# Performance work log

Measured on AMD Instinct MI355X. Metric: run time of the kernel, lower is better.

## Reference

```python
import jax, jax.numpy as jnp
import numpy as np

B = 262144
N_FEAT = 256
N_D = 64
N_A = 64
N_OUT = N_D + N_A  # 128
N_STEPS = 3
N_STEP_DEP = 2
VBS = 1024
GAMMA = 1.3
EPS_BN = 1e-5
SQRT_HALF = float(np.sqrt(0.5))


def _xavier(key, shape):
    fan_in, fan_out = shape[-2], shape[-1]
    return (jax.random.normal(key, shape) * np.sqrt(2.0 / (fan_in + fan_out))).astype(jnp.float32)


def setup_inputs() -> dict:
    key = jax.random.key(0)
    ks = jax.random.split(key, 8)
    return {
        "x": jax.random.normal(ks[0], (B, N_FEAT), dtype=jnp.float32),
        "bn0_g": jnp.ones((N_FEAT,), jnp.float32),
        "bn0_b": jnp.zeros((N_FEAT,), jnp.float32),
        "W_sh0": _xavier(ks[1], (N_FEAT, 2 * N_OUT)),
        "g_sh0": jnp.ones((2 * N_OUT,), jnp.float32),
        "b_sh0": jnp.zeros((2 * N_OUT,), jnp.float32),
        "W_sh1": _xavier(ks[2], (N_OUT, 2 * N_OUT)),
        "g_sh1": jnp.ones((2 * N_OUT,), jnp.float32),
        "b_sh1": jnp.zeros((2 * N_OUT,), jnp.float32),
        "W_step": _xavier(ks[3], (N_STEPS, N_STEP_DEP, N_OUT, 2 * N_OUT)),
        "g_step": jnp.ones((N_STEPS, N_STEP_DEP, 2 * N_OUT), jnp.float32),
        "b_step": jnp.zeros((N_STEPS, N_STEP_DEP, 2 * N_OUT), jnp.float32),
        "W_att": _xavier(ks[4], (N_STEPS, N_A, N_FEAT)),
        "g_att": jnp.ones((N_STEPS, N_FEAT), jnp.float32),
        "b_att": jnp.zeros((N_STEPS, N_FEAT), jnp.float32),
    }


def batch_norm(x, g, b):
    # training-mode BN over the full batch (biased variance, as torch)
    mu = x.mean(0)
    var = ((x - mu) ** 2).mean(0)
    return (x - mu) * jax.lax.rsqrt(var + EPS_BN) * g + b


def ghost_bn(x, g, b):
    # split batch into virtual sub-batches of VBS and BN each chunk
    n, f = x.shape
    xr = x.reshape(n // VBS, VBS, f)
    mu = xr.mean(1, keepdims=True)
    var = ((xr - mu) ** 2).mean(1, keepdims=True)
    xn = (xr - mu) * jax.lax.rsqrt(var + EPS_BN)
    return xn.reshape(n, f) * g + b


def sparsemax(z):
    zs = jnp.flip(jnp.sort(z, axis=-1), axis=-1)      # descending
    cs = jnp.cumsum(zs, axis=-1)
    n = z.shape[-1]
    k = jnp.arange(1, n + 1, dtype=z.dtype)
    support = (k * zs > cs - 1.0).astype(z.dtype)
    kz = support.sum(-1, keepdims=True)
    idx = jnp.clip(kz - 1.0, 0.0).astype(jnp.int32)
    tau = (jnp.take_along_axis(cs, idx, axis=-1) - 1.0) / kz
    return jnp.maximum(z - tau, 0.0)


def glu(x, W, g, b):
    h = ghost_bn(x @ W, g, b)
    h1, h2 = jnp.split(h, 2, axis=-1)
    return h1 * jax.nn.sigmoid(h2)


def feat_transformer(x, W_sh0, g_sh0, b_sh0, W_sh1, g_sh1, b_sh1, Wst, gst, bst):
    h = glu(x, W_sh0, g_sh0, b_sh0)
    h = (h + glu(h, W_sh1, g_sh1, b_sh1)) * SQRT_HALF
    for j in range(N_STEP_DEP):
        h = (h + glu(h, Wst[j], gst[j], bst[j])) * SQRT_HALF
    return h


def reference(x, bn0_g, bn0_b, W_sh0, g_sh0, b_sh0, W_sh1, g_sh1, b_sh1,
              W_step, g_step, b_step, W_att, g_att, b_att):
    x_bn = batch_norm(x, bn0_g, bn0_b)
    prior = jnp.ones((B, N_FEAT), x.dtype)
    h_a = jnp.zeros((B, N_A), x.dtype)
    d_out = jnp.zeros((B, N_D), x.dtype)
    sl = jnp.asarray(0.0, x.dtype)
    masks = []
    for s in range(N_STEPS):
        a = ghost_bn(h_a @ W_att[s], g_att[s], b_att[s])
        M = sparsemax(prior * a)
        masks.append(M)
        prior = prior * (GAMMA - M)
        h = feat_transformer(M * x_bn, W_sh0, g_sh0, b_sh0, W_sh1, g_sh1, b_sh1,
                             W_step[s], g_step[s], b_step[s])
        d_out = d_out + jax.nn.relu(h[:, :N_D])
        h_a = h[:, N_D:]
        sl = sl + (-M * jnp.log(M + 1e-15)).mean()
    sl = sl / N_STEPS
    return d_out, sl, jnp.stack(masks)
```

## Files before the change

### kernel.cpp

```cpp
#include <hip/hip_runtime.h>
#include <math.h>

#define B_ROWS 262144
#define GAMMA_C 1.3f
#define EPS_C 1e-5f
#define SQH_C 0.70710678118654752440f
#define SL_SCALE (1.0f/201326592.0f)

typedef _Float16 f16;
typedef f16 f16x8 __attribute__((ext_vector_type(8)));
typedef float f32x4 __attribute__((ext_vector_type(4)));

template<int RB>
__device__ __forceinline__ unsigned swz(int row, int kb) {
  constexpr int M = (RB/16 - 1) < 31 ? (RB/16 - 1) : 31;
  return (unsigned)(row * RB + (kb ^ ((row & M) << 4)));
}

__global__ void bn0_accum(const float* __restrict__ x, float* __restrict__ sums) {
  const int col = threadIdx.x;
  const size_t r0 = (size_t)blockIdx.x * 128;
  float s1 = 0.f, s2 = 0.f;
  for (int i = 0; i < 128; ++i) {
    float v = x[(r0 + i) * 256 + col];
    s1 += v; s2 += v * v;
  }
  atomicAdd(&sums[col * 2], s1);
  atomicAdd(&sums[col * 2 + 1], s2);
}

__global__ void bn0_final(const float* __restrict__ sums, const float* __restrict__ g,
                          const float* __restrict__ b, float* __restrict__ bnA,
                          float* __restrict__ bnB) {
  int c = threadIdx.x;
  float mu = sums[c * 2] * (1.f / B_ROWS);
  float var = sums[c * 2 + 1] * (1.f / B_ROWS) - mu * mu;
  float a = rsqrtf(var + EPS_C) * g[c];
  bnA[c] = a;
  bnB[c] = b[c] - mu * a;
}

__global__ void wprep(const float* __restrict__ src, f16* __restrict__ dst, int K) {
  int idx = blockIdx.x * 256 + threadIdx.x;
  int n = idx / K, k = idx - n * K;
  dst[idx] = (f16)src[(size_t)k * 256 + n];
}

__global__ void m0_kernel(const float* __restrict__ ba, float* __restrict__ m0v,
                          float* __restrict__ prior1v, float* __restrict__ slpart) {
  const int l = threadIdx.x;
  const int c0 = l << 2;
  float z[4];
#pragma unroll
  for (int j = 0; j < 4; ++j) z[j] = ba[c0 + j];
  float m = fmaxf(fmaxf(z[0], z[1]), fmaxf(z[2], z[3]));
#pragma unroll
  for (int d = 1; d < 64; d <<= 1) m = fmaxf(m, __shfl_xor(m, d));
  float lo = m - 1.f, hi = m;
  for (int it = 0; it < 24; ++it) {
    float tau = 0.5f * (lo + hi);
    float s = fmaxf(z[0] - tau, 0.f) + fmaxf(z[1] - tau, 0.f) +
              fmaxf(z[2] - tau, 0.f) + fmaxf(z[3] - tau, 0.f);
#pragma unroll
    for (int d = 1; d < 64; d <<= 1) s += __shfl_xor(s, d);
    if (s > 1.f) lo = tau; else hi = tau;
  }
  const float tau = 0.5f * (lo + hi);
  float ent = 0.f;
#pragma unroll
  for (int j = 0; j < 4; ++j) {
    float M = fmaxf(z[j] - tau, 0.f);
    m0v[c0 + j] = M;
    prior1v[c0 + j] = GAMMA_C - M;
    ent -= M * __logf(M + 1e-15f);
  }
#pragma unroll
  for (int d = 1; d < 64; d <<= 1) ent += __shfl_xor(ent, d);
  if (l == 0) slpart[512] = ent * (262144.f * SL_SCALE);
}

__global__ void mx0_kernel(const float* __restrict__ x, const float* __restrict__ m0v,
                           const float* __restrict__ bnA, const float* __restrict__ bnB,
                           float* __restrict__ mk, f16* __restrict__ Mx) {
  __shared__ float sm[256], sa[256], sb[256];
  const int tid = threadIdx.x;
  sm[tid] = m0v[tid]; sa[tid] = bnA[tid]; sb[tid] = bnB[tid];
  __syncthreads();
  const size_t r = (size_t)blockIdx.x * 8 + (tid >> 5);
  const int c0 = (tid & 31) << 3;
  const float* xp = x + r * 256 + c0;
  f32x4 x0 = *(const f32x4*)xp;
  f32x4 x1 = *(const f32x4*)(xp + 4);
  float* mp = mk + r * 256 + c0;
  f16x8 mxv;
#pragma unroll
  for (int j = 0; j < 4; ++j) {
    mp[j] = sm[c0 + j];
    mp[4 + j] = sm[c0 + 4 + j];
    mxv[j] = (f16)(sm[c0 + j] * (x0[j] * sa[c0 + j] + sb[c0 + j]));
    mxv[4 + j] = (f16)(sm[c0 + 4 + j] * (x1[j] * sa[c0 + 4 + j] + sb[c0 + 4 + j]));
  }
  *(f16x8*)(Mx + r * 256 + c0) = mxv;
}

template <int KDIM, int VARIANT>
__launch_bounds__(1024)
__global__ void fused_glu(const f16* __restrict__ Ag, const f16* __restrict__ Wt,
                          const float* __restrict__ gv, const float* __restrict__ bv,
                          f16* __restrict__ ho, float* __restrict__ dout,
                          int first, int writeH) {
  constexpr int RC  = (KDIM == 128) ? 64 : 32;
  constexpr int NCH = 1024 / RC;
  constexpr int NRT = RC / 32;
  constexpr int KS  = KDIM / 32;
  constexpr int RB  = KDIM * 2;
  constexpr int TPR = KDIM / 8;
  __shared__ f16 sW[256 * KDIM];
  __shared__ f16 sA[RC * KDIM];
  __shared__ float sS1[256], sS2[256], sAf[256], sBf[256];
  char* sWc = (char*)sW;
  char* sAc = (char*)sA;
  const int tid = threadIdx.x;
  const int r0 = blockIdx.x << 10;
  const int w = tid >> 6, l = tid & 63, lc = l & 15, lg = l >> 4;
  const int mw = w >> 3, nw = w & 7;
  if (tid < 256) { sS1[tid] = 0.f; sS2[tid] = 0.f; }
#pragma unroll
  for (int it = 0; it < KDIM / 32; ++it) {
    int flat = it * 1024 + tid;
    int rw = flat / TPR, kc = flat % TPR;
    *(f16x8*)(sWc + swz<RB>(rw, kc * 16)) = *(const f16x8*)(Wt + rw * KDIM + kc * 8);
  }
  const int arow = tid / TPR, akc = tid % TPR;
  const f16* aB = Ag + (size_t)(r0 + arow) * KDIM + akc * 8;

  for (int pass = 0; pass < 2; ++pass) {
    float st1[2] = {0.f, 0.f}, st2[2] = {0.f, 0.f};
    f16x8 pv = *(const f16x8*)(aB);
    for (int ch = 0; ch < NCH; ++ch) {
      __syncthreads();
      *(f16x8*)(sAc + swz<RB>(arow, akc * 16)) = pv;
      __syncthreads();
      if (ch + 1 < NCH) pv = *(const f16x8*)(aB + (size_t)(ch + 1) * RC * KDIM);
      f32x4 acc[NRT][2];
#pragma unroll
      for (int i = 0; i < NRT; ++i) {
        acc[i][0] = {0.f, 0.f, 0.f, 0.f};
        acc[i][1] = {0.f, 0.f, 0.f, 0.f};
      }
#pragma unroll
      for (int ks = 0; ks < KS; ++ks) {
        f16x8 af[NRT];
#pragma unroll
        for (int i = 0; i < NRT; ++i)
          af[i] = *(const f16x8*)(sAc + swz<RB>(mw * 16 * NRT + i * 16 + lc, ks * 64 + lg * 16));
        f16x8 b0 = *(const f16x8*)(sWc + swz<RB>(nw * 16 + lc, ks * 64 + lg * 16));
        f16x8 b1 = *(const f16x8*)(sWc + swz<RB>((nw + 8) * 16 + lc, ks * 64 + lg * 16));
#pragma unroll
        for (int i = 0; i < NRT; ++i) {
          acc[i][0] = __builtin_amdgcn_mfma_f32_16x16x32_f16(af[i], b0, acc[i][0], 0, 0, 0);
          acc[i][1] = __builtin_amdgcn_mfma_f32_16x16x32_f16(af[i], b1, acc[i][1], 0, 0, 0);
        }
      }
      if (pass == 0) {
#pragma unroll
        for (int t = 0; t < 2; ++t) {
          float s1 = 0.f, s2 = 0.f;
#pragma unroll
          for (int i = 0; i < NRT; ++i)
#pragma unroll
            for (int j = 0; j < 4; ++j) { float v = acc[i][t][j]; s1 += v; s2 += v * v; }
          st1[t] += s1; st2[t] += s2;
        }
      } else {
        const int c1 = nw * 16 + lc;
        const float a1 = sAf[c1], o1 = sBf[c1], a2 = sAf[c1 + 128], o2 = sBf[c1 + 128];
#pragma unroll
        for (int i = 0; i < NRT; ++i) {
          const int rloc = mw * 16 * NRT + i * 16 + lg * 4;
          const size_t rg = (size_t)(r0 + ch * RC) + rloc;
#pragma unroll
          for (int j = 0; j < 4; ++j) {
            float g1 = acc[i][0][j] * a1 + o1;
            float g2 = acc[i][1][j] * a2 + o2;
            float hv = g1 / (1.f + __expf(-g2));
            if (VARIANT >= 1) {
              f16 hp = *(const f16*)(sAc + swz<RB>(rloc + j, c1 * 2));
              hv = (hv + (float)hp) * SQH_C;
            }
            if (VARIANT < 2 || writeH) ho[(rg + j) * 128 + c1] = (f16)hv;
            if (VARIANT == 2 && nw < 4) {
              float rl = fmaxf(hv, 0.f);
              float* dp = dout + (rg + j) * 64 + c1;
              *dp = first ? rl : (*dp + rl);
            }
          }
        }
      }
    }
    if (pass == 0) {
#pragma unroll
      for (int t = 0; t < 2; ++t) {
        float v1 = st1[t], v2 = st2[t];
        v1 += __shfl_xor(v1, 16); v2 += __shfl_xor(v2, 16);
        v1 += __shfl_xor(v1, 32); v2 += __shfl_xor(v2, 32);
        if (l < 16) {
          int c = (nw + t * 8) * 16 + lc;
          atomicAdd(&sS1[c], v1);
          atomicAdd(&sS2[c], v2);
        }
      }
      __syncthreads();
      if (tid < 256) {
        float mu = sS1[tid] * (1.f / 1024.f);
        float var = sS2[tid] * (1.f / 1024.f) - mu * mu;
        float a = rsqrtf(var + EPS_C) * gv[tid];
        sAf[tid] = a;
        sBf[tid] = bv[tid] - mu * a;
      }
    }
  }
}

template <int SMODE>
__launch_bounds__(512)
__global__ void attmask(const f16* __restrict__ h1, const f16* __restrict__ Wt,
                        const float* __restrict__ ga, const float* __restrict__ ba,
                        const float* __restrict__ bnA, const float* __restrict__ bnB,
                        const float* __restrict__ prior1v, const f16* __restrict__ prin,
                        f16* __restrict__ prout, const float* __restrict__ x,
                        float* __restrict__ mk, f16* __restrict__ Mx,
                        float* __restrict__ slpart) {
  __shared__ f16 sW[256 * 64];
  __shared__ f16 sA[128 * 64];
  __shared__ float sS1[256], sS2[256], sAf[256], sBf[256], sbA[256], sbB[256], spv[256];
  __shared__ float sEnt[8];
  char* sWc = (char*)sW;
  char* sAc = (char*)sA;
  const int tid = threadIdx.x;
  const int vb = blockIdx.x;
  const int r0 = vb << 10;
  const int w = tid >> 6, l = tid & 63, lc = l & 15, lg = l >> 4;
  if (tid < 256) {
    sS1[tid] = 0.f; sS2[tid] = 0.f;
    sbA[tid] = bnA[tid]; sbB[tid] = bnB[tid];
    if (SMODE == 1) spv[tid] = prior1v[tid];
  }
#pragma unroll
  for (int it = 0; it < 4; ++it) {
    int flat = it * 512 + tid;
    int rw = flat >> 3, kc = flat & 7;
    *(f16x8*)(sWc + swz<128>(rw, kc * 16)) = *(const f16x8*)(Wt + rw * 64 + kc * 8);
  }
  const int arow = tid >> 3, akc = tid & 7;
  const f16* aB = h1 + (size_t)(r0 + arow) * 128 + 64 + akc * 8;
  float ent = 0.f;

  for (int pass = 0; pass < 2; ++pass) {
    float st1[16], st2[16];
#pragma unroll
    for (int t = 0; t < 16; ++t) { st1[t] = 0.f; st2[t] = 0.f; }
    f16x8 pv0 = *(const f16x8*)(aB);
    f16x8 pv1 = *(const f16x8*)(aB + (size_t)64 * 128);
    for (int ch = 0; ch < 8; ++ch) {
      __syncthreads();
      *(f16x8*)(sAc + swz<128>(arow, akc * 16)) = pv0;
      *(f16x8*)(sAc + swz<128>(arow + 64, akc * 16)) = pv1;
      __syncthreads();
      if (ch + 1 < 8) {
        pv0 = *(const f16x8*)(aB + (size_t)(ch + 1) * 128 * 128);
        pv1 = *(const f16x8*)(aB + (size_t)((ch + 1) * 128 + 64) * 128);
      }
      f16x8 af0 = *(const f16x8*)(sAc + swz<128>(w * 16 + lc, lg * 16));
      f16x8 af1 = *(const f16x8*)(sAc + swz<128>(w * 16 + lc, 64 + lg * 16));
      const int rb = r0 + ch * 128 + w * 16;
      f32x4 z[16];
#pragma unroll
      for (int t = 0; t < 16; ++t) {
        f16x8 b0 = *(const f16x8*)(sWc + swz<128>(t * 16 + lc, lg * 16));
        f16x8 b1 = *(const f16x8*)(sWc + swz<128>(t * 16 + lc, 64 + lg * 16));
        f32x4 acc = {0.f, 0.f, 0.f, 0.f};
        acc = __builtin_amdgcn_mfma_f32_16x16x32_f16(af0, b0, acc, 0, 0, 0);
        acc = __builtin_amdgcn_mfma_f32_16x16x32_f16(af1, b1, acc, 0, 0, 0);
        if (pass == 0) {
          float s1 = 0.f, s2 = 0.f;
#pragma unroll
          for (int j = 0; j < 4; ++j) { float v = acc[j]; s1 += v; s2 += v * v; }
          st1[t] += s1; st2[t] += s2;
        } else {
          const int c = t * 16 + lc;
          const float a = sAf[c], bb = sBf[c];
#pragma unroll
          for (int j = 0; j < 4; ++j) {
            float pr;
            if (SMODE == 1) pr = spv[c];
            else pr = (float)prin[(size_t)(rb + lg * 4 + j) * 256 + c];
            z[t][j] = (acc[j] * a + bb) * pr;
          }
        }
      }
      if (pass == 1) {
        f32x4 mj, lo, hi;
#pragma unroll
        for (int j = 0; j < 4; ++j) {
          float m = z[0][j];
#pragma unroll
          for (int t = 1; t < 16; ++t) m = fmaxf(m, z[t][j]);
          mj[j] = m;
        }
#pragma unroll
        for (int d = 1; d < 16; d <<= 1)
#pragma unroll
          for (int j = 0; j < 4; ++j) mj[j] = fmaxf(mj[j], __shfl_xor(mj[j], d));
#pragma unroll
        for (int j = 0; j < 4; ++j) { lo[j] = mj[j] - 1.f; hi[j] = mj[j]; }
        for (int itb = 0; itb < 20; ++itb) {
          f32x4 tau, sv;
#pragma unroll
          for (int j = 0; j < 4; ++j) { tau[j] = 0.5f * (lo[j] + hi[j]); sv[j] = 0.f; }
#pragma unroll
          for (int t = 0; t < 16; ++t)
#pragma unroll
            for (int j = 0; j < 4; ++j) sv[j] += fmaxf(z[t][j] - tau[j], 0.f);
#pragma unroll
          for (int d = 1; d < 16; d <<= 1)
#pragma unroll
            for (int j = 0; j < 4; ++j) sv[j] += __shfl_xor(sv[j], d);
#pragma unroll
          for (int j = 0; j < 4; ++j) { if (sv[j] > 1.f) lo[j] = tau[j]; else hi[j] = tau[j]; }
        }
        f32x4 tau;
#pragma unroll
        for (int j = 0; j < 4; ++j) tau[j] = 0.5f * (lo[j] + hi[j]);
#pragma unroll
        for (int t = 0; t < 16; ++t) {
          const int c = t * 16 + lc;
#pragma unroll
          for (int j = 0; j < 4; ++j) {
            const size_t r = (size_t)(rb + lg * 4 + j);
            float Mv = fmaxf(z[t][j] - tau[j], 0.f);
            mk[r * 256 + c] = Mv;
            ent -= Mv * __logf(Mv + 1e-15f);
            float xb = x[r * 256 + c] * sbA[c] + sbB[c];
            Mx[r * 256 + c] = (f16)(Mv * xb);
            if (SMODE == 1) prout[r * 256 + c] = (f16)(spv[c] * (GAMMA_C - Mv));
          }
        }
      }
    }
    if (pass == 0) {
#pragma unroll
      for (int t = 0; t < 16; ++t) {
        float v1 = st1[t], v2 = st2[t];
        v1 += __shfl_xor(v1, 16); v2 += __shfl_xor(v2, 16);
        v1 += __shfl_xor(v1, 32); v2 += __shfl_xor(v2, 32);
        if (l < 16) {
          atomicAdd(&sS1[t * 16 + lc], v1);
          atomicAdd(&sS2[t * 16 + lc], v2);
        }
      }
      __syncthreads();
      if (tid < 256) {
        float mu = sS1[tid] * (1.f / 1024.f);
        float var = sS2[tid] * (1.f / 1024.f) - mu * mu;
        float a = rsqrtf(var + EPS_C) * ga[tid];
        sAf[tid] = a;
        sBf[tid] = ba[tid] - mu * a;
      }
    }
  }
#pragma unroll
  for (int d = 1; d < 64; d <<= 1) ent += __shfl_xor(ent, d);
  if (l == 0) sEnt[w] = ent;
  __syncthreads();
  if (tid == 0) {
    float t = 0.f;
#pragma unroll
    for (int i = 0; i < 8; ++i) t += sEnt[i];
    slpart[(SMODE - 1) * 256 + vb] = t * SL_SCALE;
  }
}

__global__ void sl_reduce(const float* __restrict__ part, float* __restrict__ out, int n) {
  __shared__ float sm[256];
  float s = 0.f;
  for (int i = threadIdx.x; i < n; i += 256) s += part[i];
  sm[threadIdx.x] = s;
  __syncthreads();
  for (int d = 128; d > 0; d >>= 1) {
    if ((int)threadIdx.x < d) sm[threadIdx.x] += sm[threadIdx.x + d];
    __syncthreads();
  }
  if (threadIdx.x == 0) out[0] = sm[0];
}

extern "C" void kernel_launch(void* const* d_in, const int* in_sizes, int n_in,
                              void* d_out, int out_size, void* d_ws, size_t ws_size,
                              hipStream_t stream) {
  (void)in_sizes; (void)n_in; (void)out_size; (void)ws_size;
  const float* x    = (const float*)d_in[0];
  const float* bn0g = (const float*)d_in[1];
  const float* bn0b = (const float*)d_in[2];
  const float* Wsh0 = (const float*)d_in[3];
  const float* gsh0 = (const float*)d_in[4];
  const float* bsh0 = (const float*)d_in[5];
  const float* Wsh1 = (const float*)d_in[6];
  const float* gsh1 = (const float*)d_in[7];
  const float* bsh1 = (const float*)d_in[8];
  const float* Wstep = (const float*)d_in[9];
  const float* gstep = (const float*)d_in[10];
  const float* bstep = (const float*)d_in[11];
  const float* Watt = (const float*)d_in[12];
  const float* gatt = (const float*)d_in[13];
  const float* batt = (const float*)d_in[14];

  float* dout = (float*)d_out;
  float* slo = dout + (size_t)B_ROWS * 64;
  float* masks = slo + 1;

  char* ws = (char*)d_ws;
  size_t off = 0;
  auto carve = [&](size_t bytes) -> char* {
    char* p = ws + off;
    off += (bytes + 255) & ~(size_t)255;
    return p;
  };
  f16* wt_att   = (f16*)carve((size_t)3 * 256 * 64 * 2);
  f16* wt_sh0   = (f16*)carve((size_t)256 * 256 * 2);
  f16* wt_sh1   = (f16*)carve((size_t)256 * 128 * 2);
  f16* wt_step  = (f16*)carve((size_t)6 * 256 * 128 * 2);
  float* bn0sum = (float*)carve(512 * 4);
  float* bnA    = (float*)carve(256 * 4);
  float* bnB    = (float*)carve(256 * 4);
  float* m0v    = (float*)carve(256 * 4);
  float* prior1v= (float*)carve(256 * 4);
  float* slpart = (float*)carve(513 * 4);
  f16* prior    = (f16*)carve((size_t)B_ROWS * 256 * 2);
  f16* Mx       = (f16*)carve((size_t)B_ROWS * 256 * 2);
  f16* h0       = (f16*)carve((size_t)B_ROWS * 128 * 2);
  f16* h1       = (f16*)carve((size_t)B_ROWS * 128 * 2);

  hipMemsetAsync(bn0sum, 0, 512 * 4, stream);
  bn0_accum<<<2048, 256, 0, stream>>>(x, bn0sum);
  bn0_final<<<1, 256, 0, stream>>>(bn0sum, bn0g, bn0b, bnA, bnB);
  for (int s = 1; s < 3; ++s)
    wprep<<<64, 256, 0, stream>>>(Watt + (size_t)s * 64 * 256, wt_att + (size_t)s * 256 * 64, 64);
  wprep<<<256, 256, 0, stream>>>(Wsh0, wt_sh0, 256);
  wprep<<<128, 256, 0, stream>>>(Wsh1, wt_sh1, 128);
  for (int i = 0; i < 6; ++i)
    wprep<<<128, 256, 0, stream>>>(Wstep + (size_t)i * 128 * 256, wt_step + (size_t)i * 256 * 128, 128);
  m0_kernel<<<1, 64, 0, stream>>>(batt, m0v, prior1v, slpart);
  mx0_kernel<<<B_ROWS / 8, 256, 0, stream>>>(x, m0v, bnA, bnB, masks, Mx);

  for (int s = 0; s < 3; ++s) {
    if (s == 1)
      attmask<1><<<256, 512, 0, stream>>>(h1, wt_att + (size_t)1 * 256 * 64,
                                          gatt + 256, batt + 256, bnA, bnB,
                                          prior1v, nullptr, prior, x,
                                          masks + (size_t)1 * B_ROWS * 256, Mx, slpart);
    else if (s == 2)
      attmask<2><<<256, 512, 0, stream>>>(h1, wt_att + (size_t)2 * 256 * 64,
                                          gatt + 512, batt + 512, bnA, bnB,
                                          nullptr, prior, nullptr, x,
                                          masks + (size_t)2 * B_ROWS * 256, Mx, slpart);
    fused_glu<256, 0><<<256, 1024, 0, stream>>>(Mx, wt_sh0, gsh0, bsh0, h0, nullptr, 0, 1);
    fused_glu<128, 1><<<256, 1024, 0, stream>>>(h0, wt_sh1, gsh1, bsh1, h1, nullptr, 0, 1);
    fused_glu<128, 1><<<256, 1024, 0, stream>>>(h1, wt_step + (size_t)(s * 2 + 0) * 256 * 128,
                                                gstep + (s * 2 + 0) * 256, bstep + (s * 2 + 0) * 256,
                                                h0, nullptr, 0, 1);
    fused_glu<128, 2><<<256, 1024, 0, stream>>>(h0, wt_step + (size_t)(s * 2 + 1) * 256 * 128,
                                                gstep + (s * 2 + 1) * 256, bstep + (s * 2 + 1) * 256,
                                                h1, dout, s == 0, s < 2);
  }
  sl_reduce<<<1, 256, 0, stream>>>(slpart, slo, 513);
}
```

Baseline: 1.902 ms.

## Keep GLU weight fragments in registers and tile A in 64-row chunks

The fused GLU kernel now loads each wave's weight B-fragments straight from global memory into registers once, so it no longer stages the full weight matrix in LDS. That frees LDS, allowing a 64-row A tile for both K=256 and K=128 and a launch-bounds occupancy hint. The BN statistic reduction replaces shared atomics with per-half partial slots. It also adds a missing barrier in attmask and always writes h on the last step. The costs are higher register pressure, and the K=256 variant with 1024 threads may spill.

```diff
diff --git a/kernel.cpp b/kernel.cpp
--- a/kernel.cpp
+++ b/kernel.cpp
@@ -9,12 +9,11 @@
 
 typedef _Float16 f16;
 typedef f16 f16x8 __attribute__((ext_vector_type(8)));
+typedef f16 f16x4 __attribute__((ext_vector_type(4)));
 typedef float f32x4 __attribute__((ext_vector_type(4)));
 
-template<int RB>
-__device__ __forceinline__ unsigned swz(int row, int kb) {
-  constexpr int M = (RB/16 - 1) < 31 ? (RB/16 - 1) : 31;
-  return (unsigned)(row * RB + (kb ^ ((row & M) << 4)));
+__device__ __forceinline__ int SWZ(int row, int kb, int RB, int MSK) {
+  return row * RB + (kb ^ ((row & MSK) << 4));
 }
 
 __global__ void bn0_accum(const float* __restrict__ x, float* __restrict__ sums) {
@@ -103,120 +102,126 @@
   *(f16x8*)(Mx + r * 256 + c0) = mxv;
 }
 
-template <int KDIM, int VARIANT>
-__launch_bounds__(1024)
-__global__ void fused_glu(const f16* __restrict__ Ag, const f16* __restrict__ Wt,
-                          const float* __restrict__ gv, const float* __restrict__ bv,
-                          f16* __restrict__ ho, float* __restrict__ dout,
-                          int first, int writeH) {
-  constexpr int RC  = (KDIM == 128) ? 64 : 32;
-  constexpr int NCH = 1024 / RC;
-  constexpr int NRT = RC / 32;
-  constexpr int KS  = KDIM / 32;
-  constexpr int RB  = KDIM * 2;
-  constexpr int TPR = KDIM / 8;
-  __shared__ f16 sW[256 * KDIM];
-  __shared__ f16 sA[RC * KDIM];
-  __shared__ float sS1[256], sS2[256], sAf[256], sBf[256];
-  char* sWc = (char*)sW;
+template <int KD, int RESID, int DOUT>
+__launch_bounds__(1024, 4)
+__global__ void fglu(const f16* __restrict__ Ag, const f16* __restrict__ Wt,
+                     const float* __restrict__ gv, const float* __restrict__ bv,
+                     f16* __restrict__ ho, float* __restrict__ dout, int s) {
+  constexpr int KS = KD / 32;
+  constexpr int RB = KD * 2;
+  constexpr int MSK = (RB / 16 - 1) < 31 ? (RB / 16 - 1) : 31;
+  constexpr int SPT = (KD == 256) ? 2 : 1;
+  constexpr int TPR = KD / 8;
+  __shared__ __align__(16) f16 sA[64 * KD];
+  __shared__ float sS1[512], sS2[512], sAf[256], sBf[256];
   char* sAc = (char*)sA;
   const int tid = threadIdx.x;
+  const int w = tid >> 6, l = tid & 63, lg = l >> 4, lc = l & 15;
+  const int mw = w >> 3, nw = w & 7;
+  const int c1 = nw * 16 + lc, c2 = c1 + 128;
   const int r0 = blockIdx.x << 10;
-  const int w = tid >> 6, l = tid & 63, lc = l & 15, lg = l >> 4;
-  const int mw = w >> 3, nw = w & 7;
-  if (tid < 256) { sS1[tid] = 0.f; sS2[tid] = 0.f; }
-#pragma unroll
-  for (int it = 0; it < KDIM / 32; ++it) {
-    int flat = it * 1024 + tid;
-    int rw = flat / TPR, kc = flat % TPR;
-    *(f16x8*)(sWc + swz<RB>(rw, kc * 16)) = *(const f16x8*)(Wt + rw * KDIM + kc * 8);
-  }
-  const int arow = tid / TPR, akc = tid % TPR;
-  const f16* aB = Ag + (size_t)(r0 + arow) * KDIM + akc * 8;
-
-  for (int pass = 0; pass < 2; ++pass) {
-    float st1[2] = {0.f, 0.f}, st2[2] = {0.f, 0.f};
-    f16x8 pv = *(const f16x8*)(aB);
-    for (int ch = 0; ch < NCH; ++ch) {
-      __syncthreads();
-      *(f16x8*)(sAc + swz<RB>(arow, akc * 16)) = pv;
-      __syncthreads();
-      if (ch + 1 < NCH) pv = *(const f16x8*)(aB + (size_t)(ch + 1) * RC * KDIM);
-      f32x4 acc[NRT][2];
-#pragma unroll
-      for (int i = 0; i < NRT; ++i) {
-        acc[i][0] = {0.f, 0.f, 0.f, 0.f};
-        acc[i][1] = {0.f, 0.f, 0.f, 0.f};
-      }
+
+  f16x8 bf0[KS], bf1[KS];
+#pragma unroll
+  for (int ks = 0; ks < KS; ++ks) {
+    bf0[ks] = *(const f16x8*)(Wt + (size_t)c1 * KD + ks * 32 + lg * 8);
+    bf1[ks] = *(const f16x8*)(Wt + (size_t)c2 * KD + ks * 32 + lg * 8);
+  }
+
+  f16x8 pv[SPT];
+  auto LDA = [&](int ch) {
+#pragma unroll
+    for (int p = 0; p < SPT; ++p) {
+      int flat = p * 1024 + tid;
+      int row = flat / TPR, kc = flat % TPR;
+      pv[p] = *(const f16x8*)(Ag + (size_t)(r0 + ch * 64 + row) * KD + kc * 8);
+    }
+  };
+  auto STA = [&]() {
+#pragma unroll
+    for (int p = 0; p < SPT; ++p) {
+      int flat = p * 1024 + tid;
+      int row = flat / TPR, kc = flat % TPR;
+      *(f16x8*)(sAc + SWZ(row, kc * 16, RB, MSK)) = pv[p];
+    }
+  };
+
+  float st1a = 0.f, st2a = 0.f, st1b = 0.f, st2b = 0.f;
+  LDA(0);
+  for (int ch = 0; ch < 16; ++ch) {
+    __syncthreads();
+    STA();
+    __syncthreads();
+    if (ch < 15) LDA(ch + 1);
+#pragma unroll
+    for (int mt = 0; mt < 2; ++mt) {
+      f32x4 a0 = {0.f,0.f,0.f,0.f}, a1 = {0.f,0.f,0.f,0.f};
+      const int ar = mw * 32 + mt * 16 + lc;
 #pragma unroll
       for (int ks = 0; ks < KS; ++ks) {
-        f16x8 af[NRT];
-#pragma unroll
-        for (int i = 0; i < NRT; ++i)
-          af[i] = *(const f16x8*)(sAc + swz<RB>(mw * 16 * NRT + i * 16 + lc, ks * 64 + lg * 16));
-        f16x8 b0 = *(const f16x8*)(sWc + swz<RB>(nw * 16 + lc, ks * 64 + lg * 16));
-        f16x8 b1 = *(const f16x8*)(sWc + swz<RB>((nw + 8) * 16 + lc, ks * 64 + lg * 16));
-#pragma unroll
-        for (int i = 0; i < NRT; ++i) {
-          acc[i][0] = __builtin_amdgcn_mfma_f32_16x16x32_f16(af[i], b0, acc[i][0], 0, 0, 0);
-          acc[i][1] = __builtin_amdgcn_mfma_f32_16x16x32_f16(af[i], b1, acc[i][1], 0, 0, 0);
-        }
-      }
-      if (pass == 0) {
-#pragma unroll
-        for (int t = 0; t < 2; ++t) {
-          float s1 = 0.f, s2 = 0.f;
-#pragma unroll
-          for (int i = 0; i < NRT; ++i)
-#pragma unroll
-            for (int j = 0; j < 4; ++j) { float v = acc[i][t][j]; s1 += v; s2 += v * v; }
-          st1[t] += s1; st2[t] += s2;
-        }
-      } else {
-        const int c1 = nw * 16 + lc;
-        const float a1 = sAf[c1], o1 = sBf[c1], a2 = sAf[c1 + 128], o2 = sBf[c1 + 128];
-#pragma unroll
-        for (int i = 0; i < NRT; ++i) {
-          const int rloc = mw * 16 * NRT + i * 16 + lg * 4;
-          const size_t rg = (size_t)(r0 + ch * RC) + rloc;
-#pragma unroll
-          for (int j = 0; j < 4; ++j) {
-            float g1 = acc[i][0][j] * a1 + o1;
-            float g2 = acc[i][1][j] * a2 + o2;
-            float hv = g1 / (1.f + __expf(-g2));
-            if (VARIANT >= 1) {
-              f16 hp = *(const f16*)(sAc + swz<RB>(rloc + j, c1 * 2));
-              hv = (hv + (float)hp) * SQH_C;
-            }
-            if (VARIANT < 2 || writeH) ho[(rg + j) * 128 + c1] = (f16)hv;
-            if (VARIANT == 2 && nw < 4) {
-              float rl = fmaxf(hv, 0.f);
-              float* dp = dout + (rg + j) * 64 + c1;
-              *dp = first ? rl : (*dp + rl);
-            }
-          }
-        }
-      }
-    }
-    if (pass == 0) {
-#pragma unroll
-      for (int t = 0; t < 2; ++t) {
-        float v1 = st1[t], v2 = st2[t];
-        v1 += __shfl_xor(v1, 16); v2 += __shfl_xor(v2, 16);
-        v1 += __shfl_xor(v1, 32); v2 += __shfl_xor(v2, 32);
-        if (l < 16) {
-          int c = (nw + t * 8) * 16 + lc;
-          atomicAdd(&sS1[c], v1);
-          atomicAdd(&sS2[c], v2);
-        }
-      }
-      __syncthreads();
-      if (tid < 256) {
-        float mu = sS1[tid] * (1.f / 1024.f);
-        float var = sS2[tid] * (1.f / 1024.f) - mu * mu;
-        float a = rsqrtf(var + EPS_C) * gv[tid];
-        sAf[tid] = a;
-        sBf[tid] = bv[tid] - mu * a;
+        f16x8 af = *(const f16x8*)(sAc + SWZ(ar, ks * 64 + lg * 16, RB, MSK));
+        a0 = __builtin_amdgcn_mfma_f32_16x16x32_f16(af, bf0[ks], a0, 0, 0, 0);
+        a1 = __builtin_amdgcn_mfma_f32_16x16x32_f16(af, bf1[ks], a1, 0, 0, 0);
+      }
+#pragma unroll
+      for (int j = 0; j < 4; ++j) {
+        st1a += a0[j]; st2a += a0[j] * a0[j];
+        st1b += a1[j]; st2b += a1[j] * a1[j];
+      }
+    }
+  }
+  st1a += __shfl_xor(st1a, 16); st1a += __shfl_xor(st1a, 32);
+  st2a += __shfl_xor(st2a, 16); st2a += __shfl_xor(st2a, 32);
+  st1b += __shfl_xor(st1b, 16); st1b += __shfl_xor(st1b, 32);
+  st2b += __shfl_xor(st2b, 16); st2b += __shfl_xor(st2b, 32);
+  if (l < 16) {
+    sS1[mw * 256 + c1] = st1a; sS2[mw * 256 + c1] = st2a;
+    sS1[mw * 256 + c2] = st1b; sS2[mw * 256 + c2] = st2b;
+  }
+  __syncthreads();
+  if (tid < 256) {
+    float s1 = sS1[tid] + sS1[256 + tid];
+    float s2 = sS2[tid] + sS2[256 + tid];
+    float mu = s1 * (1.f / 1024.f);
+    float var = s2 * (1.f / 1024.f) - mu * mu;
+    float a = rsqrtf(var + EPS_C) * gv[tid];
+    sAf[tid] = a; sBf[tid] = bv[tid] - mu * a;
+  }
+  __syncthreads();
+  const float bA1 = sAf[c1], bO1 = sBf[c1], bA2 = sAf[c2], bO2 = sBf[c2];
+
+  LDA(0);
+  for (int ch = 0; ch < 16; ++ch) {
+    __syncthreads();
+    STA();
+    __syncthreads();
+    if (ch < 15) LDA(ch + 1);
+#pragma unroll
+    for (int mt = 0; mt < 2; ++mt) {
+      f32x4 a0 = {0.f,0.f,0.f,0.f}, a1 = {0.f,0.f,0.f,0.f};
+      const int ar = mw * 32 + mt * 16 + lc;
+#pragma unroll
+      for (int ks = 0; ks < KS; ++ks) {
+        f16x8 af = *(const f16x8*)(sAc + SWZ(ar, ks * 64 + lg * 16, RB, MSK));
+        a0 = __builtin_amdgcn_mfma_f32_16x16x32_f16(af, bf0[ks], a0, 0, 0, 0);
+        a1 = __builtin_amdgcn_mfma_f32_16x16x32_f16(af, bf1[ks], a1, 0, 0, 0);
+      }
+#pragma unroll
+      for (int j = 0; j < 4; ++j) {
+        float g1 = a0[j] * bA1 + bO1;
+        float g2 = a1[j] * bA2 + bO2;
+        float hv = g1 / (1.f + __expf(-g2));
+        const int rl = mw * 32 + mt * 16 + lg * 4 + j;
+        if (RESID) {
+          f16 hp = *(const f16*)(sAc + SWZ(rl, c1 * 2, RB, MSK));
+          hv = (hv + (float)hp) * SQH_C;
+        }
+        if (DOUT && nw < 4) {
+          float rv = fmaxf(hv, 0.f);
+          float* dp = dout + (size_t)(r0 + ch * 64 + rl) * 64 + c1;
+          if (s == 0) *dp = rv; else *dp += rv;
+        }
+        ho[(size_t)(r0 + ch * 64 + rl) * 128 + c1] = (f16)hv;
       }
     }
   }
@@ -250,7 +255,7 @@
   for (int it = 0; it < 4; ++it) {
     int flat = it * 512 + tid;
     int rw = flat >> 3, kc = flat & 7;
-    *(f16x8*)(sWc + swz<128>(rw, kc * 16)) = *(const f16x8*)(Wt + rw * 64 + kc * 8);
+    *(f16x8*)(sWc + SWZ(rw, kc * 16, 128, 7)) = *(const f16x8*)(Wt + rw * 64 + kc * 8);
   }
   const int arow = tid >> 3, akc = tid & 7;
   const f16* aB = h1 + (size_t)(r0 + arow) * 128 + 64 + akc * 8;
@@ -264,21 +269,21 @@
     f16x8 pv1 = *(const f16x8*)(aB + (size_t)64 * 128);
     for (int ch = 0; ch < 8; ++ch) {
       __syncthreads();
-      *(f16x8*)(sAc + swz<128>(arow, akc * 16)) = pv0;
-      *(f16x8*)(sAc + swz<128>(arow + 64, akc * 16)) = pv1;
+      *(f16x8*)(sAc + SWZ(arow, akc * 16, 128, 7)) = pv0;
+      *(f16x8*)(sAc + SWZ(arow + 64, akc * 16, 128, 7)) = pv1;
       __syncthreads();
       if (ch + 1 < 8) {
         pv0 = *(const f16x8*)(aB + (size_t)(ch + 1) * 128 * 128);
         pv1 = *(const f16x8*)(aB + (size_t)((ch + 1) * 128 + 64) * 128);
       }
-      f16x8 af0 = *(const f16x8*)(sAc + swz<128>(w * 16 + lc, lg * 16));
-      f16x8 af1 = *(const f16x8*)(sAc + swz<128>(w * 16 + lc, 64 + lg * 16));
+      f16x8 af0 = *(const f16x8*)(sAc + SWZ(w * 16 + lc, lg * 16, 128, 7));
+      f16x8 af1 = *(const f16x8*)(sAc + SWZ(w * 16 + lc, 64 + lg * 16, 128, 7));
       const int rb = r0 + ch * 128 + w * 16;
       f32x4 z[16];
 #pragma unroll
       for (int t = 0; t < 16; ++t) {
-        f16x8 b0 = *(const f16x8*)(sWc + swz<128>(t * 16 + lc, lg * 16));
-        f16x8 b1 = *(const f16x8*)(sWc + swz<128>(t * 16 + lc, 64 + lg * 16));
+        f16x8 b0 = *(const f16x8*)(sWc + SWZ(t * 16 + lc, lg * 16, 128, 7));
+        f16x8 b1 = *(const f16x8*)(sWc + SWZ(t * 16 + lc, 64 + lg * 16, 128, 7));
         f32x4 acc = {0.f, 0.f, 0.f, 0.f};
         acc = __builtin_amdgcn_mfma_f32_16x16x32_f16(af0, b0, acc, 0, 0, 0);
         acc = __builtin_amdgcn_mfma_f32_16x16x32_f16(af1, b1, acc, 0, 0, 0);
@@ -367,6 +372,7 @@
         sAf[tid] = a;
         sBf[tid] = ba[tid] - mu * a;
       }
+      __syncthreads();
     }
   }
 #pragma unroll
@@ -463,14 +469,14 @@
                                           gatt + 512, batt + 512, bnA, bnB,
                                           nullptr, prior, nullptr, x,
                                           masks + (size_t)2 * B_ROWS * 256, Mx, slpart);
-    fused_glu<256, 0><<<256, 1024, 0, stream>>>(Mx, wt_sh0, gsh0, bsh0, h0, nullptr, 0, 1);
-    fused_glu<128, 1><<<256, 1024, 0, stream>>>(h0, wt_sh1, gsh1, bsh1, h1, nullptr, 0, 1);
-    fused_glu<128, 1><<<256, 1024, 0, stream>>>(h1, wt_step + (size_t)(s * 2 + 0) * 256 * 128,
-                                                gstep + (s * 2 + 0) * 256, bstep + (s * 2 + 0) * 256,
-                                                h0, nullptr, 0, 1);
-    fused_glu<128, 2><<<256, 1024, 0, stream>>>(h0, wt_step + (size_t)(s * 2 + 1) * 256 * 128,
-                                                gstep + (s * 2 + 1) * 256, bstep + (s * 2 + 1) * 256,
-                                                h1, dout, s == 0, s < 2);
+    fglu<256, 0, 0><<<256, 1024, 0, stream>>>(Mx, wt_sh0, gsh0, bsh0, h0, nullptr, s);
+    fglu<128, 1, 0><<<256, 1024, 0, stream>>>(h0, wt_sh1, gsh1, bsh1, h1, nullptr, s);
+    fglu<128, 1, 0><<<256, 1024, 0, stream>>>(h1, wt_step + (size_t)(s * 2 + 0) * 256 * 128,
+                                              gstep + (s * 2 + 0) * 256, bstep + (s * 2 + 0) * 256,
+                                              h0, nullptr, s);
+    fglu<128, 1, 1><<<256, 1024, 0, stream>>>(h0, wt_step + (size_t)(s * 2 + 1) * 256 * 128,
+                                              gstep + (s * 2 + 1) * 256, bstep + (s * 2 + 1) * 256,
+                                              h1, dout, s);
   }
   sl_reduce<<<1, 256, 0, stream>>>(slpart, slo, 513);
 }
```

Result: no change. 1.908 ms (+0.3%).
